# Optimization experiments

Hardware: AMD Instinct MI355X
Metric: run time of the kernel (lower is better)

## Reference

```python
import jax, jax.numpy as jnp
import numpy as np

POOLED_H = 7
POOLED_W = 7
SPATIAL_SCALE = 0.0625
B, C, H, W = 8, 256, 48, 48
R = 300
IMG = 768  # = H / SPATIAL_SCALE


def setup_inputs() -> dict:
    key = jax.random.key(0)
    k1, k2, k3, k4 = jax.random.split(key, 4)
    features = jax.random.normal(k1, (B, C, H, W), dtype=jnp.float32)
    # rois: (batch_idx, x1, y1, x2, y2) in input-image coords
    bidx = jax.random.randint(k2, (R, 1), 0, B).astype(jnp.float32)
    tl = jax.random.uniform(k3, (R, 2), minval=0.0, maxval=IMG - 64.0)
    wh = jax.random.uniform(k4, (R, 2), minval=32.0, maxval=320.0)
    br = jnp.minimum(tl + wh, IMG - 1.0)
    rois = jnp.concatenate([bidx, tl, br], axis=1).astype(jnp.float32)
    return {"features": features, "rois": rois}


def _hat_integral(x, grid):
    """Integral from -inf to x of the unit hat basis function centered at each
    grid point g (support [g-1, g+1], peak 1, total mass 1).
    x: [..., 1-broadcastable], grid: [G] -> returns [..., G]."""
    t = x[..., None] - (grid - 1.0)
    return jnp.where(
        t <= 0.0, 0.0,
        jnp.where(t <= 1.0, 0.5 * t * t,
                  jnp.where(t <= 2.0, 1.0 - 0.5 * (2.0 - t) ** 2, 1.0)))


def reference(features, rois):
    # Precise RoI Pooling: exact double integral of the bilinear interpolant
    # over each bin, divided by bin area. Bilinear interp (with zero padding
    # outside the map, as in the CUDA PrRoIPoolingGetData) is
    #   f(u,v) = sum_{j,i} feat[j,i] * hat_j(v) * hat_i(u)
    # so the bin integral factorizes into per-axis hat-integral weights.
    Bf, Cf, Hf, Wf = features.shape
    bidx = rois[:, 0].astype(jnp.int32)
    x1 = rois[:, 1] * SPATIAL_SCALE
    y1 = rois[:, 2] * SPATIAL_SCALE
    x2 = rois[:, 3] * SPATIAL_SCALE
    y2 = rois[:, 4] * SPATIAL_SCALE
    roi_w = jnp.maximum(x2 - x1, 0.0)
    roi_h = jnp.maximum(y2 - y1, 0.0)
    bin_w = roi_w / POOLED_W  # [R]
    bin_h = roi_h / POOLED_H

    ph = jnp.arange(POOLED_H, dtype=jnp.float32)
    pw = jnp.arange(POOLED_W, dtype=jnp.float32)
    ya = y1[:, None] + ph[None, :] * bin_h[:, None]  # [R, PH]
    yb = ya + bin_h[:, None]
    xa = x1[:, None] + pw[None, :] * bin_w[:, None]  # [R, PW]
    xb = xa + bin_w[:, None]

    gy = jnp.arange(Hf, dtype=jnp.float32)
    gx = jnp.arange(Wf, dtype=jnp.float32)
    Wy = _hat_integral(yb, gy) - _hat_integral(ya, gy)  # [R, PH, H]
    Wx = _hat_integral(xb, gx) - _hat_integral(xa, gx)  # [R, PW, W]

    feat = features[bidx]  # [R, C, H, W]
    t = jnp.einsum('rpj,rcji->rcpi', Wy, feat)   # integrate over y
    num = jnp.einsum('rqi,rcpi->rcpq', Wx, t)    # integrate over x -> [R,C,PH,PW]

    area = (bin_w * bin_h)[:, None, None, None]  # win_size per ROI
    out = jnp.where(area > 0.0, num / jnp.where(area > 0.0, area, 1.0), 0.0)
    return out
```

## Files before the change

### kernel.cpp

```cpp
#include <hip/hip_runtime.h>


#define PH 7
#define PW 7
#define NBINS 49
#define SCALE 0.0625f
#define CH 256
#define FH 48
#define FW 48
#define RNUM 300
#define CB 16
#define MAXJ 23
#define ROWF 28

__device__ __forceinline__ float hat_int(float x, float g) {
    float t = x - (g - 1.0f);
    if (t <= 0.0f) return 0.0f;
    if (t <= 1.0f) return 0.5f * t * t;
    if (t <= 2.0f) { float u = 2.0f - t; return 1.0f - 0.5f * u * u; }
    return 1.0f;
}

__global__ __launch_bounds__(256)
void prroi_fused(const float* __restrict__ feat,
                 const float* __restrict__ rois,
                 float* __restrict__ out) {
    const int cblk = blockIdx.x;
    const int r    = blockIdx.y;
    const int c0   = cblk * CB;
    const int tid  = threadIdx.x;

    __shared__ float patch[MAXJ * ROWF * CB];
    __shared__ float s_wy[PH][6];
    __shared__ float s_wx[PW][6];
    __shared__ int   s_jb[PH], s_jc[PH];
    __shared__ int   s_ib[PW], s_ic[PW];

    const float* roi = rois + r * 5;
    const int   b  = (int)roi[0];
    const float x1 = roi[1] * SCALE, y1 = roi[2] * SCALE;
    const float x2 = roi[3] * SCALE, y2 = roi[4] * SCALE;
    const float roi_w = fmaxf(x2 - x1, 0.0f), roi_h = fmaxf(y2 - y1, 0.0f);
    const float bin_w = roi_w / (float)PW, bin_h = roi_h / (float)PH;
    const float area = bin_w * bin_h;
    const float inv_area = (area > 0.0f) ? (1.0f / area) : 0.0f;

    const float ylo = fminf(y1, y2), yhi = fmaxf(y1, y2);
    const float xlo = fminf(x1, x2), xhi = fmaxf(x1, x2);
    const int j0  = max(0, (int)floorf(ylo) - 1);
    const int j1  = min(FH - 1, (int)floorf(yhi) + 1);
    const int i0  = max(0, (int)floorf(xlo) - 1);
    const int i1  = min(FW - 1, (int)floorf(xhi) + 1);
    const int i0a = i0 & ~3;
    const int jspan = j1 - j0 + 1;
    const int ni4   = ((i1 - i0a) >> 2) + 1;

    if (tid < PH + PW) {
        if (tid < PH) {
            const int ph = tid;
            const float ya = y1 + ph * bin_h, yb = ya + bin_h;
            int jb0 = max(0, (int)floorf(ya) - 1);
            int jb1 = min(FH - 1, (int)floorf(yb) + 1);
            jb0 = max(jb0, j0); jb1 = min(jb1, j1);
            s_jb[ph] = jb0 - j0;
            s_jc[ph] = jb1 - jb0 + 1;
#pragma unroll
            for (int k = 0; k < 6; ++k) {
                const float g = (float)(jb0 + k);
                s_wy[ph][k] = hat_int(yb, g) - hat_int(ya, g);
            }
        } else {
            const int pw = tid - PH;
            const float xa = x1 + pw * bin_w, xb = xa + bin_w;
            int ib0 = max(0, (int)floorf(xa) - 1);
            int ib1 = min(FW - 1, (int)floorf(xb) + 1);
            ib0 = max(ib0, i0); ib1 = min(ib1, i1);
            s_ib[pw] = ib0 - i0a;
            s_ic[pw] = ib1 - ib0 + 1;
#pragma unroll
            for (int k = 0; k < 6; ++k) {
                const float g = (float)(ib0 + k);
                s_wx[pw][k] = hat_int(xb, g) - hat_int(xa, g);
            }
        }
    }

    const float* fb = feat + (size_t)(b * CH + c0) * FH * FW;
    for (int u = tid; u < 4 * MAXJ * 7; u += 256) {
        const int q   = u / (MAXJ * 7);
        const int rem = u - q * (MAXJ * 7);
        const int j   = rem / 7;
        const int i4  = rem - j * 7;
        if (j < jspan && i4 < ni4) {
            int ig = i0a + 4 * i4;
            if (ig > FW - 4) ig = FW - 4;
            const float* src = fb + ((size_t)(4 * q) * FH + (j0 + j)) * FW + ig;
            const float4 v0 = *(const float4*)(src);
            const float4 v1 = *(const float4*)(src + FH * FW);
            const float4 v2 = *(const float4*)(src + 2 * FH * FW);
            const float4 v3 = *(const float4*)(src + 3 * FH * FW);
            float* dst = &patch[((size_t)j * ROWF + (ig - i0a)) * CB + 4 * q];
            *(float4*)(dst + 0 * CB) = make_float4(v0.x, v1.x, v2.x, v3.x);
            *(float4*)(dst + 1 * CB) = make_float4(v0.y, v1.y, v2.y, v3.y);
            *(float4*)(dst + 2 * CB) = make_float4(v0.z, v1.z, v2.z, v3.z);
            *(float4*)(dst + 3 * CB) = make_float4(v0.w, v1.w, v2.w, v3.w);
        }
    }
    __syncthreads();

    const int bin = tid >> 2;
    const int q   = tid & 3;
    if (bin < NBINS) {
        const int ph = bin / PW;
        const int pw = bin - ph * PW;
        const int jb = s_jb[ph], jc = s_jc[ph];
        const int ib = s_ib[pw], ic = s_ic[pw];
        float wy[6], wx[6];
#pragma unroll
        for (int k = 0; k < 6; ++k) { wy[k] = s_wy[ph][k]; wx[k] = s_wx[pw][k]; }

        float ax = 0.0f, ay = 0.0f, az = 0.0f, aw = 0.0f;
        const float* pc = &patch[((size_t)jb * ROWF + ib) * CB + 4 * q];
        for (int jj = 0; jj < jc; ++jj) {
            const float* prow = pc + (size_t)jj * (ROWF * CB);
            const float wyj = wy[jj];
#pragma unroll
            for (int ii = 0; ii < 6; ++ii) {
                if (ii < ic) {
                    const float w = wyj * wx[ii];
                    const float4 v = *(const float4*)(prow + ii * CB);
                    ax += w * v.x;
                    ay += w * v.y;
                    az += w * v.z;
                    aw += w * v.w;
                }
            }
        }
        float* o = out + ((size_t)r * CH + c0 + 4 * q) * NBINS + bin;
        o[0 * NBINS] = ax * inv_area;
        o[1 * NBINS] = ay * inv_area;
        o[2 * NBINS] = az * inv_area;
        o[3 * NBINS] = aw * inv_area;
    }
}

extern "C" void kernel_launch(void* const* d_in, const int* in_sizes, int n_in,
                              void* d_out, int out_size, void* d_ws, size_t ws_size,
                              hipStream_t stream) {
    const float* feat = (const float*)d_in[0];
    const float* rois = (const float*)d_in[1];
    float* out = (float*)d_out;

    prroi_fused<<<dim3(CH / CB, RNUM), 256, 0, stream>>>(feat, rois, out);
}
```

Baseline: 99.14 us.

## Separate bin integral into x-pass row sums then y-pass over shared buffer

Result: faster. 93.75 us (-5.4%).

```diff
diff --git a/kernel.cpp b/kernel.cpp
--- a/kernel.cpp
+++ b/kernel.cpp
@@ -31,10 +31,11 @@
     const int tid  = threadIdx.x;
 
     __shared__ float patch[MAXJ * ROWF * CB];
+    __shared__ float rs[PW * MAXJ * CB];
     __shared__ float s_wy[PH][6];
     __shared__ float s_wx[PW][6];
-    __shared__ int   s_jb[PH], s_jc[PH];
-    __shared__ int   s_ib[PW], s_ic[PW];
+    __shared__ int   s_bj[PH];
+    __shared__ int   s_bi[PW];
 
     const float* roi = rois + r * 5;
     const int   b  = (int)roi[0];
@@ -47,39 +48,33 @@
 
     const float ylo = fminf(y1, y2), yhi = fmaxf(y1, y2);
     const float xlo = fminf(x1, x2), xhi = fmaxf(x1, x2);
-    const int j0  = max(0, (int)floorf(ylo) - 1);
-    const int j1  = min(FH - 1, (int)floorf(yhi) + 1);
-    const int i0  = max(0, (int)floorf(xlo) - 1);
-    const int i1  = min(FW - 1, (int)floorf(xhi) + 1);
-    const int i0a = i0 & ~3;
-    const int jspan = j1 - j0 + 1;
-    const int ni4   = ((i1 - i0a) >> 2) + 1;
+    const int j1 = min(FH - 1, (int)floorf(yhi) + 1);
+    const int i1 = min(FW - 1, (int)floorf(xhi) + 1);
+    const int J0 = min(max(0, (int)floorf(ylo) - 1), FH - 6);
+    const int I0 = min(max(0, (int)floorf(xlo) - 1) & ~3, FW - 8);
+    const int JROWS = min(FH - J0, max(j1 - J0 + 1, 6));
+    int NI4 = min(((i1 - I0) >> 2) + 1, (FW - I0) >> 2);
+    NI4 = max(NI4, 2);
 
     if (tid < PH + PW) {
         if (tid < PH) {
             const int ph = tid;
             const float ya = y1 + ph * bin_h, yb = ya + bin_h;
-            int jb0 = max(0, (int)floorf(ya) - 1);
-            int jb1 = min(FH - 1, (int)floorf(yb) + 1);
-            jb0 = max(jb0, j0); jb1 = min(jb1, j1);
-            s_jb[ph] = jb0 - j0;
-            s_jc[ph] = jb1 - jb0 + 1;
+            const int base = min(max((int)floorf(ya) - 1, J0), J0 + JROWS - 6);
+            s_bj[ph] = base - J0;
 #pragma unroll
             for (int k = 0; k < 6; ++k) {
-                const float g = (float)(jb0 + k);
+                const float g = (float)(base + k);
                 s_wy[ph][k] = hat_int(yb, g) - hat_int(ya, g);
             }
         } else {
             const int pw = tid - PH;
             const float xa = x1 + pw * bin_w, xb = xa + bin_w;
-            int ib0 = max(0, (int)floorf(xa) - 1);
-            int ib1 = min(FW - 1, (int)floorf(xb) + 1);
-            ib0 = max(ib0, i0); ib1 = min(ib1, i1);
-            s_ib[pw] = ib0 - i0a;
-            s_ic[pw] = ib1 - ib0 + 1;
+            const int base = min(max((int)floorf(xa) - 1, I0), I0 + 4 * NI4 - 6);
+            s_bi[pw] = base - I0;
 #pragma unroll
             for (int k = 0; k < 6; ++k) {
-                const float g = (float)(ib0 + k);
+                const float g = (float)(base + k);
                 s_wx[pw][k] = hat_int(xb, g) - hat_int(xa, g);
             }
         }
@@ -91,15 +86,14 @@
         const int rem = u - q * (MAXJ * 7);
         const int j   = rem / 7;
         const int i4  = rem - j * 7;
-        if (j < jspan && i4 < ni4) {
-            int ig = i0a + 4 * i4;
-            if (ig > FW - 4) ig = FW - 4;
-            const float* src = fb + ((size_t)(4 * q) * FH + (j0 + j)) * FW + ig;
+        if (j < JROWS && i4 < NI4) {
+            const int ig = I0 + 4 * i4;
+            const float* src = fb + ((size_t)(4 * q) * FH + (J0 + j)) * FW + ig;
             const float4 v0 = *(const float4*)(src);
             const float4 v1 = *(const float4*)(src + FH * FW);
             const float4 v2 = *(const float4*)(src + 2 * FH * FW);
             const float4 v3 = *(const float4*)(src + 3 * FH * FW);
-            float* dst = &patch[((size_t)j * ROWF + (ig - i0a)) * CB + 4 * q];
+            float* dst = &patch[((size_t)j * ROWF + 4 * i4) * CB + 4 * q];
             *(float4*)(dst + 0 * CB) = make_float4(v0.x, v1.x, v2.x, v3.x);
             *(float4*)(dst + 1 * CB) = make_float4(v0.y, v1.y, v2.y, v3.y);
             *(float4*)(dst + 2 * CB) = make_float4(v0.z, v1.z, v2.z, v3.z);
@@ -108,33 +102,38 @@
     }
     __syncthreads();
 
-    const int bin = tid >> 2;
-    const int q   = tid & 3;
+    for (int u = tid; u < JROWS * 28; u += 256) {
+        const int j   = u / 28;
+        const int rem = u - j * 28;
+        const int pw  = rem >> 2;
+        const int q   = rem & 3;
+        const int bi  = s_bi[pw];
+        const float* base = &patch[((size_t)j * ROWF + bi) * CB + 4 * q];
+        float ax = 0.0f, ay = 0.0f, az = 0.0f, aw = 0.0f;
+#pragma unroll
+        for (int ii = 0; ii < 6; ++ii) {
+            const float w = s_wx[pw][ii];
+            const float4 v = *(const float4*)(base + ii * CB);
+            ax += w * v.x; ay += w * v.y; az += w * v.z; aw += w * v.w;
+        }
+        *(float4*)(&rs[((size_t)pw * MAXJ + j) * CB + 4 * q]) =
+            make_float4(ax, ay, az, aw);
+    }
+    __syncthreads();
+
+    const int bin = tid & 63;
+    const int q   = tid >> 6;
     if (bin < NBINS) {
         const int ph = bin / PW;
         const int pw = bin - ph * PW;
-        const int jb = s_jb[ph], jc = s_jc[ph];
-        const int ib = s_ib[pw], ic = s_ic[pw];
-        float wy[6], wx[6];
+        const int bj = s_bj[ph];
+        const float* rbase = &rs[((size_t)pw * MAXJ + bj) * CB + 4 * q];
+        float ax = 0.0f, ay = 0.0f, az = 0.0f, aw = 0.0f;
 #pragma unroll
-        for (int k = 0; k < 6; ++k) { wy[k] = s_wy[ph][k]; wx[k] = s_wx[pw][k]; }
-
-        float ax = 0.0f, ay = 0.0f, az = 0.0f, aw = 0.0f;
-        const float* pc = &patch[((size_t)jb * ROWF + ib) * CB + 4 * q];
-        for (int jj = 0; jj < jc; ++jj) {
-            const float* prow = pc + (size_t)jj * (ROWF * CB);
-            const float wyj = wy[jj];
-#pragma unroll
-            for (int ii = 0; ii < 6; ++ii) {
-                if (ii < ic) {
-                    const float w = wyj * wx[ii];
-                    const float4 v = *(const float4*)(prow + ii * CB);
-                    ax += w * v.x;
-                    ay += w * v.y;
-                    az += w * v.z;
-                    aw += w * v.w;
-                }
-            }
+        for (int jj = 0; jj < 6; ++jj) {
+            const float w = s_wy[ph][jj];
+            const float4 v = *(const float4*)(rbase + jj * CB);
+            ax += w * v.x; ay += w * v.y; az += w * v.z; aw += w * v.w;
         }
         float* o = out + ((size_t)r * CH + c0 + 4 * q) * NBINS + bin;
         o[0 * NBINS] = ax * inv_area;
```
